# Performance work log

Measured on AMD Instinct MI355X. Metric: run time of the kernel, lower is better.

Reference implementation:

```python
import jax, jax.numpy as jnp
import numpy as np

B, N_H, N_W, DIM, HEADS = 2, 64, 64, 768, 12
HINT = 1024
HIDDEN = DIM * 2       # LTRM expand_ratio = 2
K_ECA = 5              # ECA kernel for C=768: int(|log2(768)/2 + 0.5|)=5 (odd)
TH_LO, TH_HI, MIN_EDGE = 0.02, 0.98, 64


def setup_inputs() -> dict:
    key = jax.random.key(0)
    ks = jax.random.split(key, 12)
    N = N_H * N_W
    x = jax.random.normal(ks[0], (B, N, DIM), jnp.float32)
    # alpha hint: left half = uniform noise (uncertain -> edge tokens),
    # right half = binary blocks aligned to the 16px token cells (easy tokens)
    blocks = (jax.random.uniform(ks[1], (B, 1, N_H, N_W)) > 0.5).astype(jnp.float32)
    blocks_up = jnp.repeat(jnp.repeat(blocks, HINT // N_H, axis=2), HINT // N_W, axis=3)
    noise = jax.random.uniform(ks[2], (B, 1, HINT, HINT))
    col = jnp.arange(HINT)[None, None, None, :]
    alpha_hint = jnp.where(col < HINT // 2, noise, blocks_up)
    s = 0.02
    return {
        "x": x,
        "alpha_hint": alpha_hint,
        # global attention (Hiera-style patched MaskUnitAttention, q_stride=1)
        "qkv_w": jax.random.normal(ks[3], (DIM, 3 * DIM), jnp.float32) * s,
        "qkv_b": jnp.zeros((3 * DIM,), jnp.float32),
        "proj_w": jax.random.normal(ks[4], (DIM, DIM), jnp.float32) * s,
        "proj_b": jnp.zeros((DIM,), jnp.float32),
        # LTRM
        "ln_g": jnp.ones((DIM,), jnp.float32),
        "ln_b": jnp.zeros((DIM,), jnp.float32),
        "fc1_w": jax.random.normal(ks[5], (DIM, HIDDEN), jnp.float32) * s,
        "fc1_b": jnp.zeros((HIDDEN,), jnp.float32),
        "fc2_w": jax.random.normal(ks[6], (HIDDEN, DIM), jnp.float32) * s,  # zeros in ckpt; random for non-trivial math
        "fc2_b": jnp.zeros((DIM,), jnp.float32),
        "eca_w": jax.random.normal(ks[7], (K_ECA,), jnp.float32) * 0.2,
    }


def _edge_mask(alpha_hint):
    # F.interpolate(mode='area') with exact integer factor == block mean
    Bn = alpha_hint.shape[0]
    f_h, f_w = HINT // N_H, HINT // N_W
    hint = alpha_hint.reshape(Bn, N_H, f_h, N_W, f_w).mean(axis=(2, 4)).reshape(Bn, N_H * N_W)
    edge = (hint > TH_LO) & (hint < TH_HI)
    # per-batch fallback: too few edge tokens -> route everything to attention
    edge = jnp.where(edge.sum(axis=1, keepdims=True) < MIN_EDGE, True, edge)
    return edge  # [B, N] bool


def _layernorm(h, g, b, eps=1e-5):
    mu = h.mean(-1, keepdims=True)
    var = ((h - mu) ** 2).mean(-1, keepdims=True)
    return (h - mu) * jax.lax.rsqrt(var + eps) * g + b


def reference(x, alpha_hint, qkv_w, qkv_b, proj_w, proj_b,
              ln_g, ln_b, fc1_w, fc1_b, fc2_w, fc2_b, eca_w):
    Bn, N, C = x.shape
    hd = C // HEADS
    edge = _edge_mask(alpha_hint)                      # [B, N] bool

    # ---- edge path: global SDPA restricted to edge tokens (masked form of
    # the gather->attend->scatter routing: same math, edge keys only) ----
    qkv = (x @ qkv_w + qkv_b).reshape(Bn, N, 3, HEADS, hd)
    q = qkv[:, :, 0].transpose(0, 2, 1, 3)             # [B,H,N,hd]
    k = qkv[:, :, 1].transpose(0, 2, 1, 3)
    v = qkv[:, :, 2].transpose(0, 2, 1, 3)
    scores = jnp.einsum('bhqd,bhkd->bhqk', q, k) / jnp.sqrt(jnp.asarray(hd, x.dtype))
    scores = scores + jnp.where(edge[:, None, None, :], 0.0, -1e9).astype(x.dtype)
    attn = jax.nn.softmax(scores, axis=-1)
    o = jnp.einsum('bhqk,bhkd->bhqd', attn, v)
    o = o.transpose(0, 2, 1, 3).reshape(Bn, N, C)
    attn_out = x + (o @ proj_w + proj_b)               # residual around attention

    # ---- easy path: LTRM (subset of tokens -> DWConv branch skipped,
    # exactly as in LTRM.forward when N != H*W) ----
    h = _layernorm(x, ln_g, ln_b)
    h = jax.nn.gelu(h @ fc1_w + fc1_b, approximate=False)
    h = jax.nn.gelu(h, approximate=False)
    h = h @ fc2_w + fc2_b                              # [B,N,C]
    # ECA: avg-pool over the routed (easy) token set -> masked mean
    easy = ~edge
    cnt = jnp.maximum(easy.sum(axis=1).astype(x.dtype), 1.0)      # [B]
    pooled = (h * easy[..., None]).sum(axis=1) / cnt[:, None]     # [B,C]
    g = jax.lax.conv_general_dilated(
        pooled[:, None, :], eca_w.reshape(1, 1, K_ECA), (1,), 'SAME',
        dimension_numbers=('NCH', 'OIH', 'NCH'))[:, 0, :]          # [B,C]
    h = h * jax.nn.sigmoid(g)[:, None, :]
    ltrm_out = x + h

    # ---- scatter-combine ----
    return jnp.where(edge[..., None], attn_out, ltrm_out)
```

## Files before the change

kernel.cpp:

```cpp
#include <hip/hip_runtime.h>

using u16 = unsigned short;
using short8 = __attribute__((ext_vector_type(8))) short;
using f32x4 = __attribute__((ext_vector_type(4))) float;

#define NTOK 4096
#define CDIM 768
#define QKVD 2304
#define NHEAD 12

__device__ __forceinline__ u16 f2bf(float f) {
  unsigned u = __float_as_uint(f);
  u += 0x7FFFu + ((u >> 16) & 1u);
  return (u16)(u >> 16);
}
__device__ __forceinline__ float bf2f(u16 v) {
  return __uint_as_float(((unsigned)v) << 16);
}

__device__ __forceinline__ void gload_lds16(const void* g, void* l) {
  __builtin_amdgcn_global_load_lds(
      (__attribute__((address_space(1))) void*)g,
      (__attribute__((address_space(3))) void*)l, 16u, 0, 0u);
}

__device__ __forceinline__ float gelu_exact(float z) {
  return 0.5f * z * (1.0f + erff(z * 0.70710678118654752f));
}

__global__ __launch_bounds__(256) void pool_hint_kernel(
    const float* __restrict__ ah, float* __restrict__ hint)
{
  const int bid = blockIdx.x;
  const int b = bid >> 6, cr = bid & 63;
  const int t = threadIdx.x;
  const float* base = ah + ((size_t)b * 1024 + (size_t)cr * 16) * 1024;
  float s = 0.f;
#pragma unroll
  for (int pr = 0; pr < 16; ++pr) {
    float4 v = *(const float4*)(base + (size_t)pr * 1024 + t * 4);
    s += v.x + v.y + v.z + v.w;
  }
  s += __shfl_xor(s, 1);
  s += __shfl_xor(s, 2);
  if ((t & 3) == 0)
    hint[b * NTOK + cr * 64 + (t >> 2)] = s * (1.f / 256.f);
}

__global__ __launch_bounds__(1024) void finalize_edge_kernel(
    const float* __restrict__ hint, int* __restrict__ edge,
    int* __restrict__ qidx, int* __restrict__ eidx,
    int* __restrict__ cntE, int* __restrict__ cntZ)
{
  const int b = blockIdx.x, t = threadIdx.x;
  __shared__ int wsum[16];
  __shared__ int scntE, scntZ, stot;
  int bits[4]; int s = 0;
#pragma unroll
  for (int j = 0; j < 4; ++j) {
    float h = hint[b * NTOK + t * 4 + j];
    bits[j] = (h > 0.02f && h < 0.98f) ? 1 : 0;
    s += bits[j];
    qidx[b * NTOK + t * 4 + j] = -1;
    eidx[b * NTOK + t * 4 + j] = -1;
  }
  int sw = s;
#pragma unroll
  for (int d = 1; d < 64; d <<= 1) sw += __shfl_xor(sw, d);
  const int l = t & 63, w = t >> 6;
  if (l == 0) wsum[w] = sw;
  if (t == 0) { scntE = 0; scntZ = 0; }
  __syncthreads();
  if (t == 0) { int a = 0; for (int i = 0; i < 16; ++i) a += wsum[i]; stot = a; }
  __syncthreads();
  const bool fb = stot < 64;
#pragma unroll
  for (int j = 0; j < 4; ++j) {
    int e = fb ? 1 : bits[j];
    edge[b * NTOK + t * 4 + j] = e;
    if (e) {
      int p = atomicAdd(&scntE, 1);
      qidx[b * NTOK + p] = t * 4 + j;
    } else {
      int p = atomicAdd(&scntZ, 1);
      eidx[b * NTOK + p] = t * 4 + j;
    }
  }
  __syncthreads();
  if (t == 0) { cntE[b] = scntE; cntZ[b] = scntZ; }
}

__global__ __launch_bounds__(256) void ln_kernel(
    const float* __restrict__ x, const float* __restrict__ gam,
    const float* __restrict__ bet, u16* __restrict__ lnb, u16* __restrict__ xb)
{
  const int row = blockIdx.x, t = threadIdx.x;
  const float* xr = x + (size_t)row * CDIM;
  float v[3];
#pragma unroll
  for (int j = 0; j < 3; ++j) v[j] = xr[t + j * 256];
  float s = v[0] + v[1] + v[2];
  float ss = v[0] * v[0] + v[1] * v[1] + v[2] * v[2];
#pragma unroll
  for (int d = 1; d < 64; d <<= 1) { s += __shfl_xor(s, d); ss += __shfl_xor(ss, d); }
  __shared__ float red[8];
  const int l = t & 63, w = t >> 6;
  if (l == 0) { red[w * 2] = s; red[w * 2 + 1] = ss; }
  __syncthreads();
  s = red[0] + red[2] + red[4] + red[6];
  ss = red[1] + red[3] + red[5] + red[7];
  const float mu = s * (1.f / 768.f);
  const float rstd = rsqrtf(ss * (1.f / 768.f) - mu * mu + 1e-5f);
#pragma unroll
  for (int j = 0; j < 3; ++j) {
    const int cc = t + j * 256;
    lnb[(size_t)row * CDIM + cc] = f2bf((v[j] - mu) * rstd * gam[cc] + bet[cc]);
    xb[(size_t)row * CDIM + cc] = f2bf(v[j]);
  }
}

__global__ __launch_bounds__(256) void transpose_kernel(
    const float* __restrict__ in, u16* __restrict__ outp, int K, int N)
{
  __shared__ float tile[32][33];
  const int bx = blockIdx.x, by = blockIdx.y;
  const int tx = threadIdx.x & 31, ty = threadIdx.x >> 5;
#pragma unroll
  for (int j = 0; j < 32; j += 8)
    tile[ty + j][tx] = in[(size_t)(by * 32 + ty + j) * N + bx * 32 + tx];
  __syncthreads();
#pragma unroll
  for (int j = 0; j < 32; j += 8)
    outp[(size_t)(bx * 32 + ty + j) * K + by * 32 + tx] = f2bf(tile[tx][ty + j]);
}

template <int EPI, bool GATHER_A, bool SCATTER_OUT>
__global__ __launch_bounds__(256) void gemm_bt(
    const u16* __restrict__ A, const u16* __restrict__ Bt,
    const float* __restrict__ bias, const float* __restrict__ resid,
    const int* __restrict__ list, void* __restrict__ outp, int N, int K)
{
  const int bm = blockIdx.x, bn = blockIdx.y;
  const int b = bm >> 5, bmi = bm & 31;
  const int rb = bmi * 128;
  if (list[b * NTOK + rb] < 0) return;

  __shared__ __align__(16) u16 lA[128 * 32];
  __shared__ __align__(16) u16 lB[128 * 32];
  const int t = threadIdx.x;
  const int l = t & 63, w = t >> 6;
  const int g = l >> 4, c = l & 15;
  const int wr = w >> 1, wc = w & 1;

  f32x4 acc[4][4];
#pragma unroll
  for (int i = 0; i < 4; ++i)
#pragma unroll
    for (int j = 0; j < 4; ++j) acc[i][j] = f32x4{0.f, 0.f, 0.f, 0.f};

  const int srow = t >> 2;
  const int sslot = (t & 3) ^ (srow & 3);
  int ta0, ta1;
  if constexpr (GATHER_A) {
    ta0 = list[b * NTOK + rb + srow];       if (ta0 < 0) ta0 = 0;
    ta1 = list[b * NTOK + rb + 64 + srow];  if (ta1 < 0) ta1 = 0;
  } else {
    ta0 = rb + srow;
    ta1 = rb + 64 + srow;
  }
  const u16* gA0 = A + ((size_t)b * NTOK + ta0) * K + sslot * 8;
  const u16* gA1 = A + ((size_t)b * NTOK + ta1) * K + sslot * 8;
  const u16* gB0 = Bt + (size_t)(bn * 128 + srow) * K + sslot * 8;
  const u16* gB1 = Bt + (size_t)(bn * 128 + 64 + srow) * K + sslot * 8;
  char* ldA = (char*)lA + w * 1024;
  char* ldB = (char*)lB + w * 1024;

  for (int k0 = 0; k0 < K; k0 += 32) {
    __syncthreads();
    gload_lds16(gA0 + k0, ldA);
    gload_lds16(gA1 + k0, ldA + 4096);
    gload_lds16(gB0 + k0, ldB);
    gload_lds16(gB1 + k0, ldB + 4096);
    __syncthreads();
    short8 af[4], bfr[4];
#pragma unroll
    for (int mi = 0; mi < 4; ++mi) {
      int row = wr * 64 + mi * 16 + c;
      af[mi] = *(const short8*)((const char*)lA + row * 64 + ((g ^ (row & 3)) << 4));
    }
#pragma unroll
    for (int ni = 0; ni < 4; ++ni) {
      int row = wc * 64 + ni * 16 + c;
      bfr[ni] = *(const short8*)((const char*)lB + row * 64 + ((g ^ (row & 3)) << 4));
    }
#pragma unroll
    for (int mi = 0; mi < 4; ++mi)
#pragma unroll
      for (int ni = 0; ni < 4; ++ni)
        acc[mi][ni] = __builtin_amdgcn_mfma_f32_16x16x32_bf16(af[mi], bfr[ni], acc[mi][ni], 0, 0, 0);
  }

#pragma unroll
  for (int mi = 0; mi < 4; ++mi) {
#pragma unroll
    for (int ni = 0; ni < 4; ++ni) {
      const int col = bn * 128 + wc * 64 + ni * 16 + c;
      const float bv = bias[col];
      const int prow0 = rb + wr * 64 + mi * 16 + g * 4;
#pragma unroll
      for (int r = 0; r < 4; ++r) {
        float v = acc[mi][ni][r] + bv;
        int orow;
        if constexpr (SCATTER_OUT) {
          int tok = list[b * NTOK + prow0 + r];
          if (tok < 0) continue;
          orow = tok;
        } else {
          orow = prow0 + r;
        }
        const size_t idx = ((size_t)b * NTOK + orow) * N + col;
        if constexpr (EPI == 0) {
          ((u16*)outp)[idx] = f2bf(v);
        } else if constexpr (EPI == 1) {
          ((float*)outp)[idx] = v + resid[idx];
        } else if constexpr (EPI == 2) {
          ((u16*)outp)[idx] = f2bf(gelu_exact(gelu_exact(v)));
        } else {
          ((float*)outp)[idx] = v;
        }
      }
    }
  }
}

#define NSPLIT 2
__global__ __launch_bounds__(256) void flash_part_kernel(
    const u16* __restrict__ qkv, const int* __restrict__ cntE,
    u16* __restrict__ partO, float2* __restrict__ partML)
{
  const int qt = blockIdx.x;
  const int bh = blockIdx.y;
  const int sp = blockIdx.z;
  const int b = bh / NHEAD, h = bh % NHEAD;
  const int cnt = cntE[b];
  if (qt * 128 >= cnt) return;

  const int ntiles = (cnt + 63) >> 6;
  const int half = (ntiles + NSPLIT - 1) / NSPLIT;
  const int tA = sp * half;
  const int tB = min(ntiles, tA + half);

  __shared__ __align__(16) u16 lK[64 * 64];
  __shared__ __align__(16) u16 lV[64 * 64];
  __shared__ __align__(16) u16 lP[4][32 * 64];

  const int t = threadIdx.x;
  const int l = t & 63, w = t >> 6;
  const int g = l >> 4, c = l & 15;
  const size_t tokbase = (size_t)b * NTOK;

  short8 qf[2][2];
#pragma unroll
  for (int mi = 0; mi < 2; ++mi) {
    const int pos = qt * 128 + w * 32 + mi * 16 + c;
    const u16* qp = qkv + (tokbase + pos) * QKVD + h * 64;
#pragma unroll
    for (int kb = 0; kb < 2; ++kb)
      qf[mi][kb] = *(const short8*)(qp + kb * 32 + g * 8);
  }

  f32x4 oacc[2][4];
  float mrun[2][4], lrun[2][4];
#pragma unroll
  for (int mi = 0; mi < 2; ++mi) {
#pragma unroll
    for (int nd = 0; nd < 4; ++nd) oacc[mi][nd] = f32x4{0.f, 0.f, 0.f, 0.f};
#pragma unroll
    for (int r = 0; r < 4; ++r) { mrun[mi][r] = -1e30f; lrun[mi][r] = 0.f; }
  }

  u16* lPw = lP[w];

  for (int kt = tA; kt < tB; ++kt) {
    __syncthreads();
#pragma unroll
    for (int j = 0; j < 2; ++j) {
      int seg = j * 256 + t;
      int row = seg >> 3;
      int sl = (seg & 7) ^ (row & 7);
      gload_lds16(qkv + (tokbase + kt * 64 + row) * QKVD + CDIM + h * 64 + sl * 8,
                  (char*)lK + j * 4096 + w * 1024);
    }
    {
      const int kp = t & 31, db = t >> 5;
      const u16* vg = qkv + (tokbase + kt * 64 + kp * 2) * QKVD + 2 * CDIM + h * 64 + db * 8;
      union { uint4 q; u16 s[8]; } v0, v1;
      v0.q = *(const uint4*)vg;
      v1.q = *(const uint4*)(vg + QKVD);
#pragma unroll
      for (int j = 0; j < 8; ++j) {
        int d = db * 8 + j;
        unsigned pk = (unsigned)v0.s[j] | ((unsigned)v1.s[j] << 16);
        *(unsigned*)((char*)lV + d * 128 + ((kp * 4) ^ ((d & 7) << 4))) = pk;
      }
    }
    __syncthreads();

    short8 kf[4][2];
#pragma unroll
    for (int ni = 0; ni < 4; ++ni) {
      int row = ni * 16 + c;
#pragma unroll
      for (int kb = 0; kb < 2; ++kb)
        kf[ni][kb] = *(const short8*)((const char*)lK + row * 128 + (((kb * 4 + g) ^ (row & 7)) << 4));
    }
    f32x4 s[2][4];
#pragma unroll
    for (int mi = 0; mi < 2; ++mi)
#pragma unroll
      for (int ni = 0; ni < 4; ++ni) {
        f32x4 sv = f32x4{0.f, 0.f, 0.f, 0.f};
        sv = __builtin_amdgcn_mfma_f32_16x16x32_bf16(qf[mi][0], kf[ni][0], sv, 0, 0, 0);
        sv = __builtin_amdgcn_mfma_f32_16x16x32_bf16(qf[mi][1], kf[ni][1], sv, 0, 0, 0);
        s[mi][ni] = sv;
      }

    float emask[4];
#pragma unroll
    for (int ni = 0; ni < 4; ++ni)
      emask[ni] = (kt * 64 + ni * 16 + c < cnt) ? 0.f : -1e9f;

#pragma unroll
    for (int mi = 0; mi < 2; ++mi) {
      float mx[4];
#pragma unroll
      for (int r = 0; r < 4; ++r) {
        float a0 = s[mi][0][r] * 0.125f + emask[0];
        float a1 = s[mi][1][r] * 0.125f + emask[1];
        float a2 = s[mi][2][r] * 0.125f + emask[2];
        float a3 = s[mi][3][r] * 0.125f + emask[3];
        s[mi][0][r] = a0; s[mi][1][r] = a1; s[mi][2][r] = a2; s[mi][3][r] = a3;
        mx[r] = fmaxf(fmaxf(a0, a1), fmaxf(a2, a3));
      }
#pragma unroll
      for (int r = 0; r < 4; ++r)
#pragma unroll
        for (int d = 1; d < 16; d <<= 1)
          mx[r] = fmaxf(mx[r], __shfl_xor(mx[r], d));

      float alpha[4], rs[4];
#pragma unroll
      for (int r = 0; r < 4; ++r) {
        float mnew = fmaxf(mrun[mi][r], mx[r]);
        alpha[r] = __expf(mrun[mi][r] - mnew);
        mrun[mi][r] = mnew;
        float accp = 0.f;
        const int prow = mi * 16 + g * 4 + r;
#pragma unroll
        for (int ni = 0; ni < 4; ++ni) {
          float p = __expf(s[mi][ni][r] - mnew);
          accp += p;
          *(u16*)((char*)lPw + prow * 128 + (((ni * 16 + c) * 2) ^ ((prow & 7) << 4))) = f2bf(p);
        }
        rs[r] = accp;
      }
#pragma unroll
      for (int r = 0; r < 4; ++r)
#pragma unroll
        for (int d = 1; d < 16; d <<= 1) rs[r] += __shfl_xor(rs[r], d);
#pragma unroll
      for (int r = 0; r < 4; ++r) {
        lrun[mi][r] = lrun[mi][r] * alpha[r] + rs[r];
#pragma unroll
        for (int nd = 0; nd < 4; ++nd) oacc[mi][nd][r] *= alpha[r];
      }
    }

#pragma unroll
    for (int kb = 0; kb < 2; ++kb) {
      short8 pa[2], vf[4];
#pragma unroll
      for (int mi = 0; mi < 2; ++mi) {
        int prow = mi * 16 + c;
        pa[mi] = *(const short8*)((const char*)lPw + prow * 128 + (((kb * 4 + g) ^ (prow & 7)) << 4));
      }
#pragma unroll
      for (int nd = 0; nd < 4; ++nd) {
        int vrow = nd * 16 + c;
        vf[nd] = *(const short8*)((const char*)lV + vrow * 128 + (((kb * 4 + g) ^ (vrow & 7)) << 4));
      }
#pragma unroll
      for (int mi = 0; mi < 2; ++mi)
#pragma unroll
        for (int nd = 0; nd < 4; ++nd)
          oacc[mi][nd] = __builtin_amdgcn_mfma_f32_16x16x32_bf16(pa[mi], vf[nd], oacc[mi][nd], 0, 0, 0);
    }
  }

  const size_t pobase = ((size_t)(sp * 2 + b) * NHEAD + h) * NTOK;
#pragma unroll
  for (int mi = 0; mi < 2; ++mi) {
#pragma unroll
    for (int r = 0; r < 4; ++r) {
      const int pos = qt * 128 + w * 32 + mi * 16 + g * 4 + r;
      if (pos < cnt) {
        u16* op = partO + (pobase + pos) * 64;
#pragma unroll
        for (int nd = 0; nd < 4; ++nd)
          op[nd * 16 + c] = f2bf(oacc[mi][nd][r]);
        if (c == 0)
          partML[pobase + pos] = make_float2(mrun[mi][r], lrun[mi][r]);
      }
    }
  }
}

__global__ __launch_bounds__(256) void flash_merge_kernel(
    const u16* __restrict__ partO, const float2* __restrict__ partML,
    const int* __restrict__ cntE, u16* __restrict__ obf)
{
  const int bh = blockIdx.y;
  const int b = bh / NHEAD, h = bh % NHEAD;
  const int t = threadIdx.x;
  const int pos = blockIdx.x * 4 + (t >> 6);
  const int d = t & 63;
  if (pos >= cntE[b]) return;
  const size_t p0 = ((size_t)(0 * 2 + b) * NHEAD + h) * NTOK + pos;
  const size_t p1 = ((size_t)(1 * 2 + b) * NHEAD + h) * NTOK + pos;
  const float2 ml0 = partML[p0];
  const float2 ml1 = partML[p1];
  const float M = fmaxf(ml0.x, ml1.x);
  const float e0 = __expf(ml0.x - M);
  const float e1 = __expf(ml1.x - M);
  const float L = ml0.y * e0 + ml1.y * e1;
  const float o = (e0 * bf2f(partO[p0 * 64 + d]) + e1 * bf2f(partO[p1 * 64 + d])) / L;
  obf[((size_t)b * NTOK + pos) * CDIM + h * 64 + d] = f2bf(o);
}

__global__ __launch_bounds__(256) void pool_partial_kernel(
    const float* __restrict__ h2, const int* __restrict__ edge, float* __restrict__ pooled)
{
  const int bid = blockIdx.x;
  const int b = bid / 48, rm = bid % 48;
  const int cg = rm / 16, ts = rm % 16;
  const int ch = cg * 256 + threadIdx.x;
  float s = 0.f;
  for (int tok = ts * 256; tok < ts * 256 + 256; ++tok) {
    if (!edge[b * NTOK + tok])
      s += h2[((size_t)b * NTOK + tok) * CDIM + ch];
  }
  atomicAdd(&pooled[b * CDIM + ch], s);
}

__global__ void eca_kernel(const float* __restrict__ pooled, const float* __restrict__ w5,
                           const int* __restrict__ ecnt, float* __restrict__ gate)
{
  const int b = blockIdx.x, c = threadIdx.x;
  const float inv = 1.f / fmaxf((float)ecnt[b], 1.f);
  float a = 0.f;
#pragma unroll
  for (int j = 0; j < 5; ++j) {
    int i = c - 2 + j;
    if (i >= 0 && i < CDIM) a += w5[j] * pooled[b * CDIM + i];
  }
  a *= inv;
  gate[b * CDIM + c] = 1.f / (1.f + __expf(-a));
}

__global__ __launch_bounds__(256) void combine_kernel(
    const float* __restrict__ x, const float* __restrict__ attn,
    const float* __restrict__ h2, const float* __restrict__ gate,
    const int* __restrict__ edge, float* __restrict__ out)
{
  const size_t i = ((size_t)blockIdx.x * 256 + threadIdx.x) * 4;
  const int b = (int)(i / ((size_t)NTOK * CDIM));
  const size_t r = i % ((size_t)NTOK * CDIM);
  const int tok = (int)(r / CDIM);
  const int cc = (int)(r % CDIM);
  float4 ov;
  if (edge[b * NTOK + tok]) {
    ov = *(const float4*)(attn + i);
  } else {
    float4 xv = *(const float4*)(x + i);
    float4 hv = *(const float4*)(h2 + i);
    float4 gv = *(const float4*)(gate + b * CDIM + cc);
    ov.x = xv.x + hv.x * gv.x;
    ov.y = xv.y + hv.y * gv.y;
    ov.z = xv.z + hv.z * gv.z;
    ov.w = xv.w + hv.w * gv.w;
  }
  *(float4*)(out + i) = ov;
}

extern "C" void kernel_launch(void* const* d_in, const int* in_sizes, int n_in,
                              void* d_out, int out_size, void* d_ws, size_t ws_size,
                              hipStream_t stream) {
  const float* x      = (const float*)d_in[0];
  const float* ah     = (const float*)d_in[1];
  const float* qkv_w  = (const float*)d_in[2];
  const float* qkv_b  = (const float*)d_in[3];
  const float* proj_w = (const float*)d_in[4];
  const float* proj_b = (const float*)d_in[5];
  const float* ln_g   = (const float*)d_in[6];
  const float* ln_b   = (const float*)d_in[7];
  const float* fc1_w  = (const float*)d_in[8];
  const float* fc1_b  = (const float*)d_in[9];
  const float* fc2_w  = (const float*)d_in[10];
  const float* fc2_b  = (const float*)d_in[11];
  const float* eca_w  = (const float*)d_in[12];
  float* out = (float*)d_out;

  char* ws = (char*)d_ws;
  size_t off = 0;
  auto alloc = [&](size_t bytes) {
    char* p = ws + off;
    off += (bytes + 255) & ~(size_t)255;
    return p;
  };
  float* hint   = (float*)alloc((size_t)2 * NTOK * 4);
  int*   edge   = (int*)alloc((size_t)2 * NTOK * 4);
  int*   qidx   = (int*)alloc((size_t)2 * NTOK * 4);
  int*   eidx   = (int*)alloc((size_t)2 * NTOK * 4);
  int*   cntE   = (int*)alloc(256);
  int*   cntZ   = (int*)alloc(256);
  u16*   xbf    = (u16*)alloc((size_t)2 * NTOK * CDIM * 2);
  u16*   lnbf   = (u16*)alloc((size_t)2 * NTOK * CDIM * 2);
  u16*   qkvT   = (u16*)alloc((size_t)QKVD * CDIM * 2);
  u16*   projT  = (u16*)alloc((size_t)CDIM * CDIM * 2);
  u16*   fc1T   = (u16*)alloc((size_t)1536 * CDIM * 2);
  u16*   fc2T   = (u16*)alloc((size_t)CDIM * 1536 * 2);
  u16*   qkvb   = (u16*)alloc((size_t)2 * NTOK * QKVD * 2);
  u16*   obf    = (u16*)alloc((size_t)2 * NTOK * CDIM * 2);
  u16*   h1bf   = (u16*)alloc((size_t)2 * NTOK * 1536 * 2);
  float* h2     = (float*)alloc((size_t)2 * NTOK * CDIM * 4);
  float* attn   = (float*)alloc((size_t)2 * NTOK * CDIM * 4);
  u16*   partO  = (u16*)alloc((size_t)NSPLIT * 2 * NHEAD * NTOK * 64 * 2);
  float* partML = (float*)alloc((size_t)NSPLIT * 2 * NHEAD * NTOK * 8);
  float* pooled = (float*)alloc((size_t)2 * CDIM * 4);
  float* gate   = (float*)alloc((size_t)2 * CDIM * 4);

  pool_hint_kernel<<<dim3(128), 256, 0, stream>>>(ah, hint);
  finalize_edge_kernel<<<dim3(2), 1024, 0, stream>>>(hint, edge, qidx, eidx, cntE, cntZ);
  ln_kernel<<<dim3(8192), 256, 0, stream>>>(x, ln_g, ln_b, lnbf, xbf);
  transpose_kernel<<<dim3(72, 24), 256, 0, stream>>>(qkv_w, qkvT, 768, 2304);
  transpose_kernel<<<dim3(24, 24), 256, 0, stream>>>(proj_w, projT, 768, 768);
  transpose_kernel<<<dim3(48, 24), 256, 0, stream>>>(fc1_w, fc1T, 768, 1536);
  transpose_kernel<<<dim3(24, 48), 256, 0, stream>>>(fc2_w, fc2T, 1536, 768);

  gemm_bt<0, true, false><<<dim3(64, 18), 256, 0, stream>>>(
      xbf, qkvT, qkv_b, nullptr, qidx, qkvb, 2304, 768);
  flash_part_kernel<<<dim3(32, 24, NSPLIT), 256, 0, stream>>>(qkvb, cntE, partO, (float2*)partML);
  flash_merge_kernel<<<dim3(1024, 24), 256, 0, stream>>>(partO, (const float2*)partML, cntE, obf);
  gemm_bt<1, false, true><<<dim3(64, 6), 256, 0, stream>>>(
      obf, projT, proj_b, x, qidx, attn, 768, 768);
  gemm_bt<2, true, false><<<dim3(64, 12), 256, 0, stream>>>(
      lnbf, fc1T, fc1_b, nullptr, eidx, h1bf, 1536, 768);
  gemm_bt<3, false, true><<<dim3(64, 6), 256, 0, stream>>>(
      h1bf, fc2T, fc2_b, nullptr, eidx, h2, 768, 1536);

  hipMemsetAsync(pooled, 0, (size_t)2 * CDIM * 4, stream);
  pool_partial_kernel<<<dim3(96), 256, 0, stream>>>(h2, edge, pooled);
  eca_kernel<<<dim3(2), 768, 0, stream>>>(pooled, eca_w, cntZ, gate);
  combine_kernel<<<dim3(6144), 256, 0, stream>>>(x, attn, h2, gate, edge, out);
}
```

Before: 542.3 us.

## Double-buffer K/V in flash attention, transpose scores, use exp2, merge transposes

The flash attention partial kernel now double-buffers K and V tiles in LDS, prefetching the next tile while computing the current one, which removes one barrier per iteration. It computes S transposed (K·Q) so each lane owns a single query row, which cuts the row-max and row-sum shuffles and lets P be written as packed 8-byte stores. Softmax uses exp2 with a pre-scaled log2e factor and sets MFMA priority. The four weight-transpose launches are merged into one kernel, and the merge kernel handles empty splits. Doubling the K/V buffers raises LDS use, which may lower occupancy.

```diff
diff --git a/kernel.cpp b/kernel.cpp
--- a/kernel.cpp
+++ b/kernel.cpp
@@ -8,6 +8,8 @@
 #define CDIM 768
 #define QKVD 2304
 #define NHEAD 12
+#define NSPLIT 2
+#define SCALE2 0.18033688011112042f
 
 __device__ __forceinline__ u16 f2bf(float f) {
   unsigned u = __float_as_uint(f);
@@ -16,6 +18,9 @@
 }
 __device__ __forceinline__ float bf2f(u16 v) {
   return __uint_as_float(((unsigned)v) << 16);
+}
+__device__ __forceinline__ unsigned pkbf(float a, float b) {
+  return (unsigned)f2bf(a) | ((unsigned)f2bf(b) << 16);
 }
 
 __device__ __forceinline__ void gload_lds16(const void* g, void* l) {
@@ -119,11 +124,19 @@
   }
 }
 
-__global__ __launch_bounds__(256) void transpose_kernel(
-    const float* __restrict__ in, u16* __restrict__ outp, int K, int N)
+__global__ __launch_bounds__(256) void transpose_all_kernel(
+    const float* __restrict__ qkv_w, const float* __restrict__ proj_w,
+    const float* __restrict__ fc1_w, const float* __restrict__ fc2_w,
+    u16* __restrict__ qkvT, u16* __restrict__ projT,
+    u16* __restrict__ fc1T, u16* __restrict__ fc2T)
 {
   __shared__ float tile[32][33];
-  const int bx = blockIdx.x, by = blockIdx.y;
+  int bid = blockIdx.x;
+  const float* in; u16* outp; int K, N, bx, by;
+  if (bid < 1728)      { in = qkv_w;  outp = qkvT; K = 768;  N = 2304; bx = bid % 72; by = bid / 72; }
+  else if (bid < 2304) { bid -= 1728; in = proj_w; outp = projT; K = 768;  N = 768;  bx = bid % 24; by = bid / 24; }
+  else if (bid < 3456) { bid -= 2304; in = fc1_w;  outp = fc1T; K = 768;  N = 1536; bx = bid % 48; by = bid / 48; }
+  else                 { bid -= 3456; in = fc2_w;  outp = fc2T; K = 1536; N = 768;  bx = bid % 24; by = bid / 24; }
   const int tx = threadIdx.x & 31, ty = threadIdx.x >> 5;
 #pragma unroll
   for (int j = 0; j < 32; j += 8)
@@ -233,7 +246,6 @@
   }
 }
 
-#define NSPLIT 2
 __global__ __launch_bounds__(256) void flash_part_kernel(
     const u16* __restrict__ qkv, const int* __restrict__ cntE,
     u16* __restrict__ partO, float2* __restrict__ partML)
@@ -246,17 +258,19 @@
   if (qt * 128 >= cnt) return;
 
   const int ntiles = (cnt + 63) >> 6;
-  const int half = (ntiles + NSPLIT - 1) / NSPLIT;
-  const int tA = sp * half;
-  const int tB = min(ntiles, tA + half);
-
-  __shared__ __align__(16) u16 lK[64 * 64];
-  __shared__ __align__(16) u16 lV[64 * 64];
+  const int per = (ntiles + NSPLIT - 1) / NSPLIT;
+  const int tA = sp * per;
+  const int tB = min(ntiles, tA + per);
+  if (tA >= tB) return;
+
+  __shared__ __align__(16) u16 lK[2][64 * 64];
+  __shared__ __align__(16) u16 lV[2][64 * 64];
   __shared__ __align__(16) u16 lP[4][32 * 64];
 
   const int t = threadIdx.x;
   const int l = t & 63, w = t >> 6;
   const int g = l >> 4, c = l & 15;
+  const int kp = t & 31, db = t >> 5;
   const size_t tokbase = (size_t)b * NTOK;
 
   short8 qf[2][2];
@@ -270,147 +284,165 @@
   }
 
   f32x4 oacc[2][4];
-  float mrun[2][4], lrun[2][4];
+  float m2run[2], lrun[2];
 #pragma unroll
   for (int mi = 0; mi < 2; ++mi) {
 #pragma unroll
     for (int nd = 0; nd < 4; ++nd) oacc[mi][nd] = f32x4{0.f, 0.f, 0.f, 0.f};
-#pragma unroll
-    for (int r = 0; r < 4; ++r) { mrun[mi][r] = -1e30f; lrun[mi][r] = 0.f; }
-  }
-
-  u16* lPw = lP[w];
-
-  for (int kt = tA; kt < tB; ++kt) {
-    __syncthreads();
+    m2run[mi] = -1e30f; lrun[mi] = 0.f;
+  }
+
+  char* lPw = (char*)lP[w];
+
+  auto stageK = [&](int kt, int buf) {
 #pragma unroll
     for (int j = 0; j < 2; ++j) {
       int seg = j * 256 + t;
       int row = seg >> 3;
       int sl = (seg & 7) ^ (row & 7);
       gload_lds16(qkv + (tokbase + kt * 64 + row) * QKVD + CDIM + h * 64 + sl * 8,
-                  (char*)lK + j * 4096 + w * 1024);
-    }
-    {
-      const int kp = t & 31, db = t >> 5;
-      const u16* vg = qkv + (tokbase + kt * 64 + kp * 2) * QKVD + 2 * CDIM + h * 64 + db * 8;
-      union { uint4 q; u16 s[8]; } v0, v1;
-      v0.q = *(const uint4*)vg;
-      v1.q = *(const uint4*)(vg + QKVD);
-#pragma unroll
-      for (int j = 0; j < 8; ++j) {
-        int d = db * 8 + j;
-        unsigned pk = (unsigned)v0.s[j] | ((unsigned)v1.s[j] << 16);
-        *(unsigned*)((char*)lV + d * 128 + ((kp * 4) ^ ((d & 7) << 4))) = pk;
-      }
-    }
-    __syncthreads();
-
+                  (char*)lK[buf] + j * 4096 + w * 1024);
+    }
+  };
+  uint4 va, vb;
+  auto loadV = [&](int kt) {
+    const u16* vg = qkv + (tokbase + kt * 64 + kp * 2) * QKVD + 2 * CDIM + h * 64 + db * 8;
+    va = *(const uint4*)vg;
+    vb = *(const uint4*)(vg + QKVD);
+  };
+  auto writeV = [&](int buf) {
+    union { uint4 q; u16 s[8]; } u0, u1; u0.q = va; u1.q = vb;
+    char* lvb = (char*)lV[buf];
+#pragma unroll
+    for (int j = 0; j < 8; ++j) {
+      int d = db * 8 + j;
+      unsigned pk = (unsigned)u0.s[j] | ((unsigned)u1.s[j] << 16);
+      *(unsigned*)(lvb + d * 128 + ((kp * 4) ^ ((d & 7) << 4))) = pk;
+    }
+  };
+
+  int cur = 0;
+  stageK(tA, 0);
+  loadV(tA);
+  writeV(0);
+  __syncthreads();
+
+  for (int kt = tA; kt < tB; ++kt) {
+    const bool hasNext = (kt + 1 < tB);
+    if (hasNext) { stageK(kt + 1, cur ^ 1); loadV(kt + 1); }
+
+    const char* lKc = (const char*)lK[cur];
     short8 kf[4][2];
 #pragma unroll
     for (int ni = 0; ni < 4; ++ni) {
       int row = ni * 16 + c;
 #pragma unroll
       for (int kb = 0; kb < 2; ++kb)
-        kf[ni][kb] = *(const short8*)((const char*)lK + row * 128 + (((kb * 4 + g) ^ (row & 7)) << 4));
-    }
-    f32x4 s[2][4];
+        kf[ni][kb] = *(const short8*)(lKc + row * 128 + (((kb * 4 + g) ^ (row & 7)) << 4));
+    }
+    f32x4 st[2][4];
+    __builtin_amdgcn_s_setprio(1);
 #pragma unroll
     for (int mi = 0; mi < 2; ++mi)
 #pragma unroll
       for (int ni = 0; ni < 4; ++ni) {
         f32x4 sv = f32x4{0.f, 0.f, 0.f, 0.f};
-        sv = __builtin_amdgcn_mfma_f32_16x16x32_bf16(qf[mi][0], kf[ni][0], sv, 0, 0, 0);
-        sv = __builtin_amdgcn_mfma_f32_16x16x32_bf16(qf[mi][1], kf[ni][1], sv, 0, 0, 0);
-        s[mi][ni] = sv;
+        sv = __builtin_amdgcn_mfma_f32_16x16x32_bf16(kf[ni][0], qf[mi][0], sv, 0, 0, 0);
+        sv = __builtin_amdgcn_mfma_f32_16x16x32_bf16(kf[ni][1], qf[mi][1], sv, 0, 0, 0);
+        st[mi][ni] = sv;
       }
-
-    float emask[4];
-#pragma unroll
-    for (int ni = 0; ni < 4; ++ni)
-      emask[ni] = (kt * 64 + ni * 16 + c < cnt) ? 0.f : -1e9f;
+    __builtin_amdgcn_s_setprio(0);
+
+    const int kvalid = cnt - kt * 64;
+#pragma unroll
+    for (int mi = 0; mi < 2; ++mi)
+#pragma unroll
+      for (int ni = 0; ni < 4; ++ni)
+#pragma unroll
+        for (int r = 0; r < 4; ++r) {
+          float v = st[mi][ni][r] * SCALE2;
+          st[mi][ni][r] = (ni * 16 + g * 4 + r < kvalid) ? v : -1e30f;
+        }
 
 #pragma unroll
     for (int mi = 0; mi < 2; ++mi) {
-      float mx[4];
-#pragma unroll
-      for (int r = 0; r < 4; ++r) {
-        float a0 = s[mi][0][r] * 0.125f + emask[0];
-        float a1 = s[mi][1][r] * 0.125f + emask[1];
-        float a2 = s[mi][2][r] * 0.125f + emask[2];
-        float a3 = s[mi][3][r] * 0.125f + emask[3];
-        s[mi][0][r] = a0; s[mi][1][r] = a1; s[mi][2][r] = a2; s[mi][3][r] = a3;
-        mx[r] = fmaxf(fmaxf(a0, a1), fmaxf(a2, a3));
+      float mx = fmaxf(
+          fmaxf(fmaxf(fmaxf(st[mi][0][0], st[mi][0][1]), fmaxf(st[mi][0][2], st[mi][0][3])),
+                fmaxf(fmaxf(st[mi][1][0], st[mi][1][1]), fmaxf(st[mi][1][2], st[mi][1][3]))),
+          fmaxf(fmaxf(fmaxf(st[mi][2][0], st[mi][2][1]), fmaxf(st[mi][2][2], st[mi][2][3])),
+                fmaxf(fmaxf(st[mi][3][0], st[mi][3][1]), fmaxf(st[mi][3][2], st[mi][3][3]))));
+      mx = fmaxf(mx, __shfl_xor(mx, 16));
+      mx = fmaxf(mx, __shfl_xor(mx, 32));
+      const float m2new = fmaxf(m2run[mi], mx);
+      const float alpha = exp2f(m2run[mi] - m2new);
+      m2run[mi] = m2new;
+      float rs = 0.f;
+      const int qrow = mi * 16 + c;
+      char* base = lPw + qrow * 128;
+      const int swz = (qrow & 7) << 4;
+#pragma unroll
+      for (int ni = 0; ni < 4; ++ni) {
+        float p0 = exp2f(st[mi][ni][0] - m2new);
+        float p1 = exp2f(st[mi][ni][1] - m2new);
+        float p2 = exp2f(st[mi][ni][2] - m2new);
+        float p3 = exp2f(st[mi][ni][3] - m2new);
+        rs += (p0 + p1) + (p2 + p3);
+        *(uint2*)(base + ((ni * 32 + g * 8) ^ swz)) = make_uint2(pkbf(p0, p1), pkbf(p2, p3));
       }
-#pragma unroll
-      for (int r = 0; r < 4; ++r)
-#pragma unroll
-        for (int d = 1; d < 16; d <<= 1)
-          mx[r] = fmaxf(mx[r], __shfl_xor(mx[r], d));
-
-      float alpha[4], rs[4];
-#pragma unroll
-      for (int r = 0; r < 4; ++r) {
-        float mnew = fmaxf(mrun[mi][r], mx[r]);
-        alpha[r] = __expf(mrun[mi][r] - mnew);
-        mrun[mi][r] = mnew;
-        float accp = 0.f;
-        const int prow = mi * 16 + g * 4 + r;
-#pragma unroll
-        for (int ni = 0; ni < 4; ++ni) {
-          float p = __expf(s[mi][ni][r] - mnew);
-          accp += p;
-          *(u16*)((char*)lPw + prow * 128 + (((ni * 16 + c) * 2) ^ ((prow & 7) << 4))) = f2bf(p);
-        }
-        rs[r] = accp;
+      rs += __shfl_xor(rs, 16);
+      rs += __shfl_xor(rs, 32);
+      lrun[mi] = lrun[mi] * alpha + rs;
+#pragma unroll
+      for (int nd = 0; nd < 4; ++nd)
+#pragma unroll
+        for (int r = 0; r < 4; ++r) oacc[mi][nd][r] *= alpha;
+    }
+
+    const char* lVc = (const char*)lV[cur];
+#pragma unroll
+    for (int kb = 0; kb < 2; ++kb) {
+      short8 pb[2], vf[4];
+#pragma unroll
+      for (int mi = 0; mi < 2; ++mi) {
+        int qrow = mi * 16 + c;
+        pb[mi] = *(const short8*)(lPw + qrow * 128 + (((kb * 64 + g * 16)) ^ ((qrow & 7) << 4)));
       }
 #pragma unroll
-      for (int r = 0; r < 4; ++r)
-#pragma unroll
-        for (int d = 1; d < 16; d <<= 1) rs[r] += __shfl_xor(rs[r], d);
-#pragma unroll
-      for (int r = 0; r < 4; ++r) {
-        lrun[mi][r] = lrun[mi][r] * alpha[r] + rs[r];
-#pragma unroll
-        for (int nd = 0; nd < 4; ++nd) oacc[mi][nd][r] *= alpha[r];
+      for (int nd = 0; nd < 4; ++nd) {
+        int d = nd * 16 + c;
+        vf[nd] = *(const short8*)(lVc + d * 128 + (((kb * 4 + g) ^ (d & 7)) << 4));
       }
-    }
-
-#pragma unroll
-    for (int kb = 0; kb < 2; ++kb) {
-      short8 pa[2], vf[4];
-#pragma unroll
-      for (int mi = 0; mi < 2; ++mi) {
-        int prow = mi * 16 + c;
-        pa[mi] = *(const short8*)((const char*)lPw + prow * 128 + (((kb * 4 + g) ^ (prow & 7)) << 4));
+      __builtin_amdgcn_s_setprio(1);
+#pragma unroll
+      for (int mi = 0; mi < 2; ++mi)
+#pragma unroll
+        for (int nd = 0; nd < 4; ++nd)
+          oacc[mi][nd] = __builtin_amdgcn_mfma_f32_16x16x32_bf16(vf[nd], pb[mi], oacc[mi][nd], 0, 0, 0);
+      __builtin_amdgcn_s_setprio(0);
+    }
+
+    if (hasNext) writeV(cur ^ 1);
+    __syncthreads();
+    cur ^= 1;
+  }
+
+  const size_t pobase = ((size_t)(sp * 2 + b) * NHEAD + h) * NTOK;
+#pragma unroll
+  for (int mi = 0; mi < 2; ++mi) {
+    const int pos = qt * 128 + w * 32 + mi * 16 + c;
+    if (pos < cnt) {
+      u16* op = partO + (pobase + pos) * 64;
+#pragma unroll
+      for (int nd = 0; nd < 4; ++nd) {
+        ushort4 pk4;
+        pk4.x = f2bf(oacc[mi][nd][0]);
+        pk4.y = f2bf(oacc[mi][nd][1]);
+        pk4.z = f2bf(oacc[mi][nd][2]);
+        pk4.w = f2bf(oacc[mi][nd][3]);
+        *(ushort4*)(op + nd * 16 + g * 4) = pk4;
       }
-#pragma unroll
-      for (int nd = 0; nd < 4; ++nd) {
-        int vrow = nd * 16 + c;
-        vf[nd] = *(const short8*)((const char*)lV + vrow * 128 + (((kb * 4 + g) ^ (vrow & 7)) << 4));
-      }
-#pragma unroll
-      for (int mi = 0; mi < 2; ++mi)
-#pragma unroll
-        for (int nd = 0; nd < 4; ++nd)
-          oacc[mi][nd] = __builtin_amdgcn_mfma_f32_16x16x32_bf16(pa[mi], vf[nd], oacc[mi][nd], 0, 0, 0);
-    }
-  }
-
-  const size_t pobase = ((size_t)(sp * 2 + b) * NHEAD + h) * NTOK;
-#pragma unroll
-  for (int mi = 0; mi < 2; ++mi) {
-#pragma unroll
-    for (int r = 0; r < 4; ++r) {
-      const int pos = qt * 128 + w * 32 + mi * 16 + g * 4 + r;
-      if (pos < cnt) {
-        u16* op = partO + (pobase + pos) * 64;
-#pragma unroll
-        for (int nd = 0; nd < 4; ++nd)
-          op[nd * 16 + c] = f2bf(oacc[mi][nd][r]);
-        if (c == 0)
-          partML[pobase + pos] = make_float2(mrun[mi][r], lrun[mi][r]);
-      }
+      if (g == 0)
+        partML[pobase + pos] = make_float2(m2run[mi], lrun[mi]);
     }
   }
 }
@@ -424,17 +456,32 @@
   const int t = threadIdx.x;
   const int pos = blockIdx.x * 4 + (t >> 6);
   const int d = t & 63;
-  if (pos >= cntE[b]) return;
-  const size_t p0 = ((size_t)(0 * 2 + b) * NHEAD + h) * NTOK + pos;
-  const size_t p1 = ((size_t)(1 * 2 + b) * NHEAD + h) * NTOK + pos;
-  const float2 ml0 = partML[p0];
-  const float2 ml1 = partML[p1];
-  const float M = fmaxf(ml0.x, ml1.x);
-  const float e0 = __expf(ml0.x - M);
-  const float e1 = __expf(ml1.x - M);
-  const float L = ml0.y * e0 + ml1.y * e1;
-  const float o = (e0 * bf2f(partO[p0 * 64 + d]) + e1 * bf2f(partO[p1 * 64 + d])) / L;
-  obf[((size_t)b * NTOK + pos) * CDIM + h * 64 + d] = f2bf(o);
+  const int cnt = cntE[b];
+  if (pos >= cnt) return;
+  const int ntiles = (cnt + 63) >> 6;
+  const int per = (ntiles + NSPLIT - 1) / NSPLIT;
+
+  float2 ml[NSPLIT];
+  float M = -3e38f;
+  int nact = 0;
+#pragma unroll
+  for (int sp = 0; sp < NSPLIT; ++sp) {
+    if (sp * per < ntiles) {
+      ml[sp] = partML[((size_t)(sp * 2 + b) * NHEAD + h) * NTOK + pos];
+      M = fmaxf(M, ml[sp].x);
+      nact = sp + 1;
+    }
+  }
+  float L = 0.f, O = 0.f;
+#pragma unroll
+  for (int sp = 0; sp < NSPLIT; ++sp) {
+    if (sp < nact) {
+      const float e = exp2f(ml[sp].x - M);
+      L += ml[sp].y * e;
+      O += e * bf2f(partO[(((size_t)(sp * 2 + b) * NHEAD + h) * NTOK + pos) * 64 + d]);
+    }
+  }
+  obf[((size_t)b * NTOK + pos) * CDIM + h * 64 + d] = f2bf(O / L);
 }
 
 __global__ __launch_bounds__(256) void pool_partial_kernel(
@@ -542,10 +589,8 @@
   pool_hint_kernel<<<dim3(128), 256, 0, stream>>>(ah, hint);
   finalize_edge_kernel<<<dim3(2), 1024, 0, stream>>>(hint, edge, qidx, eidx, cntE, cntZ);
   ln_kernel<<<dim3(8192), 256, 0, stream>>>(x, ln_g, ln_b, lnbf, xbf);
-  transpose_kernel<<<dim3(72, 24), 256, 0, stream>>>(qkv_w, qkvT, 768, 2304);
-  transpose_kernel<<<dim3(24, 24), 256, 0, stream>>>(proj_w, projT, 768, 768);
-  transpose_kernel<<<dim3(48, 24), 256, 0, stream>>>(fc1_w, fc1T, 768, 1536);
-  transpose_kernel<<<dim3(24, 48), 256, 0, stream>>>(fc2_w, fc2T, 1536, 768);
+  transpose_all_kernel<<<dim3(4608), 256, 0, stream>>>(
+      qkv_w, proj_w, fc1_w, fc2_w, qkvT, projT, fc1T, fc2T);
 
   gemm_bt<0, true, false><<<dim3(64, 18), 256, 0, stream>>>(
       xbf, qkvT, qkv_b, nullptr, qidx, qkvb, 2304, 768);
```

Measured after the change: 530.8 us. -2.1%, faster.
